# Performance work log

Measured on AMD Instinct MI355X. Metric: run time of the kernel, lower is better.

The kernel has to match this reference:

```python
import jax, jax.numpy as jnp
import numpy as np

B, L, NC, REG_MAX = 32, 8400, 15, 16
EPS_IOU = 0.1  # RotatedIoULoss eps (clamp min)


def _cross2(a, b):
    return a[..., 0] * b[..., 1] - a[..., 1] * b[..., 0]


def _box2corners(box):
    # box [...,5] = (x, y, w, h, alpha) -> corners [...,4,2], consistent cyclic order
    x, y, w, h, a = (box[..., i] for i in range(5))
    xo = jnp.array([0.5, -0.5, -0.5, 0.5], box.dtype)
    yo = jnp.array([-0.5, -0.5, 0.5, 0.5], box.dtype)
    px = w[..., None] * xo  # [...,4]
    py = h[..., None] * yo
    c, s = jnp.cos(a)[..., None], jnp.sin(a)[..., None]
    rx = c * px - s * py + x[..., None]
    ry = s * px + c * py + y[..., None]
    return jnp.stack([rx, ry], axis=-1)


def _box_intersection(c1, c2):
    # segment-segment intersections between the 4 edges of each box -> [N,16,2], valid [N,16]
    p1 = c1[:, :, None, :]
    p2 = jnp.roll(c1, -1, axis=-2)[:, :, None, :]
    q1 = c2[:, None, :, :]
    q2 = jnp.roll(c2, -1, axis=-2)[:, None, :, :]
    d1, d2, r = p2 - p1, q2 - q1, q1 - p1
    den = _cross2(d1, d2)
    safe = jnp.where(jnp.abs(den) < 1e-12, jnp.ones_like(den), den)
    t = _cross2(r, d2) / safe
    u = _cross2(r, d1) / safe
    valid = (jnp.abs(den) > 1e-12) & (t > 0) & (t < 1) & (u > 0) & (u < 1)
    pts = p1 + t[..., None] * d1
    pts = jnp.where(valid[..., None], pts, jnp.zeros_like(pts))
    N = c1.shape[0]
    return pts.reshape(N, 16, 2), valid.reshape(N, 16)


def _points_in_box(pts, corners):
    # pts [N,4,2] inside rotated box given by corners [N,4,2] (projection test)
    a = corners[:, 0:1]
    ab = corners[:, 1:2] - a
    ad = corners[:, 3:4] - a
    ap = pts - a
    pab = jnp.sum(ap * ab, -1)
    pad = jnp.sum(ap * ad, -1)
    nab = jnp.sum(ab * ab, -1)
    nad = jnp.sum(ad * ad, -1)
    return (pab >= 0) & (pab <= nab) & (pad >= 0) & (pad <= nad)


def _sorted_poly_area(verts, mask):
    # sort candidate vertices CCW around the centroid of valid ones, shoelace area
    mf = mask.astype(verts.dtype)
    nv = jnp.maximum(mf.sum(-1, keepdims=True), 1.0)  # [N,1]
    mean = (verts * mf[..., None]).sum(-2, keepdims=True) / nv[..., None]
    rel = verts - mean
    ang = jnp.where(mask, jnp.arctan2(rel[..., 1], rel[..., 0]), 1e6)
    order = jnp.argsort(ang, axis=-1)
    sv = jnp.take_along_axis(verts, order[..., None], axis=-2)
    sm = jnp.take_along_axis(mask, order, axis=-1)
    sv = jnp.where(sm[..., None], sv, sv[..., :1, :])  # pad invalid with first vertex
    nxt = jnp.roll(sv, -1, axis=-2)
    return 0.5 * jnp.abs(jnp.sum(sv[..., 0] * nxt[..., 1] - nxt[..., 0] * sv[..., 1], axis=-1))


def diff_iou_rotated_2d(box1, box2):
    # box1, box2: [N,5] -> iou [N]
    c1, c2 = _box2corners(box1), _box2corners(box2)
    ipts, ivalid = _box_intersection(c1, c2)
    m1 = _points_in_box(c1, c2)
    m2 = _points_in_box(c2, c1)
    verts = jnp.concatenate([c1, c2, ipts], axis=-2)   # [N,24,2]
    mask = jnp.concatenate([m1, m2, ivalid], axis=-1)  # [N,24]
    inter = _sorted_poly_area(verts, mask)
    area1 = box1[..., 2] * box1[..., 3]
    area2 = box2[..., 2] * box2[..., 3]
    return inter / (area1 + area2 - inter + 1e-9)


def setup_inputs() -> dict:
    key = jax.random.key(0)
    ks = jax.random.split(key, 8)
    wh_off = jnp.array([0.0, 0.0, 0.2, 0.2], jnp.float32)
    pred_bboxes = jax.random.uniform(ks[0], (B, L, 4), jnp.float32) + wh_off
    target_bboxes = jax.random.uniform(ks[1], (B, L, 4), jnp.float32) + wh_off
    pred_angles = 0.5 * jax.random.normal(ks[2], (B, L, 1), jnp.float32)      # radians
    target_angles = 90.0 * jax.random.uniform(ks[3], (B, L, 1), jnp.float32)  # degrees
    pred_dist = jax.random.normal(ks[4], (B, L, (REG_MAX + 1) * 4), jnp.float32)
    target_scores = jax.random.uniform(ks[5], (B, L, NC), jnp.float32)
    fg_mask = jax.random.bernoulli(ks[6], 0.25, (B, L))
    tss = jnp.sum(target_scores.sum(-1) * fg_mask.astype(jnp.float32))[None]
    anchor_points = jax.random.uniform(ks[7], (L, 2), jnp.float32)
    return {"pred_dist": pred_dist, "pred_bboxes": pred_bboxes, "pred_angles": pred_angles,
            "anchor_points": anchor_points, "target_bboxes": target_bboxes,
            "target_angles": target_angles, "target_scores": target_scores,
            "target_scores_sum": tss, "fg_mask": fg_mask}


def reference(pred_dist, pred_bboxes, pred_angles, anchor_points, target_bboxes,
              target_angles, target_scores, target_scores_sum, fg_mask):
    mf = fg_mask.astype(pred_bboxes.dtype).reshape(-1)          # [B*L]
    num_pos = mf.sum()
    pi = jnp.asarray(np.pi, pred_bboxes.dtype)
    pred_R = jnp.concatenate([pred_bboxes, pred_angles], -1).reshape(-1, 5)
    tgt_R = jnp.concatenate([target_bboxes, target_angles / 180.0 * pi], -1).reshape(-1, 5)
    ious = jnp.maximum(diff_iou_rotated_2d(pred_R, tgt_R), EPS_IOU)  # clamp(min=eps)
    bbox_weight = target_scores.sum(-1).reshape(-1)             # [B*L]
    loss_elem = (1.0 - ious) * bbox_weight * mf                 # masked per-anchor loss
    lsum = loss_elem.sum()
    lmean = lsum / jnp.maximum(num_pos, 1.0)
    loss_iou = jnp.where(target_scores_sum[0] == 0, lsum, lmean)
    loss_iou = jnp.where(num_pos > 0, loss_iou, 0.0)
    loss_dfl = pred_dist.sum() * 0.0
    return (loss_iou, loss_dfl)
```

## Files before the change

kernel.cpp:

```cpp
#include <hip/hip_runtime.h>
#include <math.h>

#define NCLS 15


__global__ void zero_ws_kernel(float* ws) {
    if (threadIdx.x < 2) ws[threadIdx.x] = 0.0f;
}

__global__ __launch_bounds__(256) void rbox_iou_kernel(
    const float* __restrict__ pred_bboxes,
    const float* __restrict__ pred_angles,
    const float* __restrict__ target_bboxes,
    const float* __restrict__ target_angles,
    const float* __restrict__ target_scores,
    const int*   __restrict__ fg_mask,
    float* __restrict__ ws,
    int n)
{
    const int i = blockIdx.x * blockDim.x + threadIdx.x;
    float loss = 0.0f, cnt = 0.0f;

    if (i < n && fg_mask[i] != 0) {
        cnt = 1.0f;

        const float4 pb = reinterpret_cast<const float4*>(pred_bboxes)[i];
        const float4 tb = reinterpret_cast<const float4*>(target_bboxes)[i];
        const float pa = pred_angles[i];
        const float ta = (target_angles[i] / 180.0f) * (float)M_PI;

        float c1x[4], c1y[4], c2x[4], c2y[4];
        {
            const float xo[4] = { 0.5f, -0.5f, -0.5f, 0.5f };
            const float yo[4] = { -0.5f, -0.5f, 0.5f, 0.5f };
            float cs = cosf(pa), sn = sinf(pa);
#pragma unroll
            for (int k = 0; k < 4; ++k) {
                float px = pb.z * xo[k], py = pb.w * yo[k];
                c1x[k] = cs * px - sn * py + pb.x;
                c1y[k] = sn * px + cs * py + pb.y;
            }
            cs = cosf(ta); sn = sinf(ta);
#pragma unroll
            for (int k = 0; k < 4; ++k) {
                float px = tb.z * xo[k], py = tb.w * yo[k];
                c2x[k] = cs * px - sn * py + tb.x;
                c2y[k] = sn * px + cs * py + tb.y;
            }
        }

        float vx[24], vy[24];
        bool  vm[24];

        {
            const float ax = c2x[0], ay = c2y[0];
            const float abx = c2x[1] - ax, aby = c2y[1] - ay;
            const float adx = c2x[3] - ax, ady = c2y[3] - ay;
            const float nab = abx * abx + aby * aby;
            const float nad = adx * adx + ady * ady;
#pragma unroll
            for (int k = 0; k < 4; ++k) {
                float apx = c1x[k] - ax, apy = c1y[k] - ay;
                float pab = apx * abx + apy * aby;
                float pad = apx * adx + apy * ady;
                vx[k] = c1x[k]; vy[k] = c1y[k];
                vm[k] = (pab >= 0.0f) && (pab <= nab) && (pad >= 0.0f) && (pad <= nad);
            }
        }
        {
            const float ax = c1x[0], ay = c1y[0];
            const float abx = c1x[1] - ax, aby = c1y[1] - ay;
            const float adx = c1x[3] - ax, ady = c1y[3] - ay;
            const float nab = abx * abx + aby * aby;
            const float nad = adx * adx + ady * ady;
#pragma unroll
            for (int k = 0; k < 4; ++k) {
                float apx = c2x[k] - ax, apy = c2y[k] - ay;
                float pab = apx * abx + apy * aby;
                float pad = apx * adx + apy * ady;
                vx[4 + k] = c2x[k]; vy[4 + k] = c2y[k];
                vm[4 + k] = (pab >= 0.0f) && (pab <= nab) && (pad >= 0.0f) && (pad <= nad);
            }
        }
#pragma unroll
        for (int a = 0; a < 4; ++a) {
            const float p1x = c1x[a], p1y = c1y[a];
            const float d1x = c1x[(a + 1) & 3] - p1x;
            const float d1y = c1y[(a + 1) & 3] - p1y;
#pragma unroll
            for (int b = 0; b < 4; ++b) {
                const float q1x = c2x[b], q1y = c2y[b];
                const float d2x = c2x[(b + 1) & 3] - q1x;
                const float d2y = c2y[(b + 1) & 3] - q1y;
                const float rx = q1x - p1x, ry = q1y - p1y;
                const float den = d1x * d2y - d1y * d2x;
                const float safe = (fabsf(den) < 1e-12f) ? 1.0f : den;
                const float t = (rx * d2y - ry * d2x) / safe;
                const float u = (rx * d1y - ry * d1x) / safe;
                const bool val = (fabsf(den) > 1e-12f) &&
                                 (t > 0.0f) && (t < 1.0f) &&
                                 (u > 0.0f) && (u < 1.0f);
                const int idx = 8 + a * 4 + b;
                vx[idx] = val ? (p1x + t * d1x) : 0.0f;
                vy[idx] = val ? (p1y + t * d1y) : 0.0f;
                vm[idx] = val;
            }
        }

        float sx = 0.0f, sy = 0.0f, nvf = 0.0f;
#pragma unroll
        for (int k = 0; k < 24; ++k) {
            sx  += vm[k] ? vx[k] : 0.0f;
            sy  += vm[k] ? vy[k] : 0.0f;
            nvf += vm[k] ? 1.0f : 0.0f;
        }
        const float nv = fmaxf(nvf, 1.0f);
        const float mx = sx / nv, my = sy / nv;

        float ang[24];
#pragma unroll
        for (int k = 0; k < 24; ++k) {
            const float rx = vx[k] - mx, ry = vy[k] - my;
            const float d = fabsf(rx) + fabsf(ry);
            const float a = rx / d;
            float p = (ry >= 0.0f) ? (1.0f - a) : (3.0f + a);
            if (d == 0.0f) p = 0.0f;
            ang[k] = vm[k] ? p : INFINITY;
        }

        float minA = INFINITY, mnx = 0.0f, mny = 0.0f;
#pragma unroll
        for (int k = 0; k < 24; ++k) {
            const bool t = ang[k] < minA;
            minA = t ? ang[k] : minA;
            mnx  = t ? vx[k]  : mnx;
            mny  = t ? vy[k]  : mny;
        }

        float total = 0.0f;
#pragma unroll
        for (int a = 0; a < 24; ++a) {
            const float ai = ang[a];
            float bestA = INFINITY;
            float bx = mnx, by = mny;
#pragma unroll
            for (int b = 0; b < 24; ++b) {
                if (b == a) continue;
                const float aj = ang[b];
                const bool gt = (b > a) ? (aj >= ai) : (aj > ai);
                const bool take = gt && (aj < bestA);
                bestA = take ? aj : bestA;
                bx = take ? vx[b] : bx;
                by = take ? vy[b] : by;
            }
            if (ai < INFINITY)
                total += vx[a] * by - bx * vy[a];
        }
        const float inter = 0.5f * fabsf(total);

        const float area1 = pb.z * pb.w;
        const float area2 = tb.z * tb.w;
        float iou = inter / (area1 + area2 - inter + 1e-9f);
        iou = fmaxf(iou, 0.1f);

        float w = 0.0f;
#pragma unroll
        for (int k = 0; k < NCLS; ++k) w += target_scores[i * NCLS + k];

        loss = (1.0f - iou) * w;
    }

#pragma unroll
    for (int off = 32; off > 0; off >>= 1) {
        loss += __shfl_down(loss, off, 64);
        cnt  += __shfl_down(cnt,  off, 64);
    }
    __shared__ float sl[4], sc[4];
    const int lane = threadIdx.x & 63;
    const int wid  = threadIdx.x >> 6;
    if (lane == 0) { sl[wid] = loss; sc[wid] = cnt; }
    __syncthreads();
    if (threadIdx.x == 0) {
        const float L = sl[0] + sl[1] + sl[2] + sl[3];
        const float C = sc[0] + sc[1] + sc[2] + sc[3];
        atomicAdd(&ws[0], L);
        atomicAdd(&ws[1], C);
    }
}

__global__ void finalize_kernel(const float* __restrict__ ws,
                                const float* __restrict__ tss,
                                float* __restrict__ out)
{
    const float lsum = ws[0];
    const float npos = ws[1];
    const float lmean = lsum / fmaxf(npos, 1.0f);
    float li = (tss[0] == 0.0f) ? lsum : lmean;
    li = (npos > 0.0f) ? li : 0.0f;
    out[0] = li;
    out[1] = 0.0f;
}

extern "C" void kernel_launch(void* const* d_in, const int* in_sizes, int n_in,
                              void* d_out, int out_size, void* d_ws, size_t ws_size,
                              hipStream_t stream) {
    const float* pred_bboxes   = (const float*)d_in[1];
    const float* pred_angles   = (const float*)d_in[2];
    const float* target_bboxes = (const float*)d_in[4];
    const float* target_angles = (const float*)d_in[5];
    const float* target_scores = (const float*)d_in[6];
    const float* tss           = (const float*)d_in[7];
    const int*   fg_mask       = (const int*)d_in[8];

    float* ws  = (float*)d_ws;
    float* out = (float*)d_out;

    const int n = in_sizes[8];
    const int blocks = (n + 255) / 256;

    zero_ws_kernel<<<1, 64, 0, stream>>>(ws);
    rbox_iou_kernel<<<blocks, 256, 0, stream>>>(
        pred_bboxes, pred_angles, target_bboxes, target_angles,
        target_scores, fg_mask, ws, n);
    finalize_kernel<<<1, 1, 0, stream>>>(ws, tss, out);
}
```

Before: 164.2 us.

## Compact foreground anchors and replace selection-based vertex ordering with bitonic sort

```diff
diff --git a/kernel.cpp b/kernel.cpp
--- a/kernel.cpp
+++ b/kernel.cpp
@@ -2,11 +2,50 @@
 #include <math.h>
 
 #define NCLS 15
+#define NV 24
 
 
 __global__ void zero_ws_kernel(float* ws) {
-    if (threadIdx.x < 2) ws[threadIdx.x] = 0.0f;
-}
+    if (threadIdx.x == 0) { ws[0] = 0.0f; ((int*)ws)[1] = 0; }
+}
+
+__global__ __launch_bounds__(256) void compact_kernel(
+    const int* __restrict__ fg_mask, int n,
+    int* __restrict__ cnt, int* __restrict__ idxbuf)
+{
+    const int i = blockIdx.x * 256 + threadIdx.x;
+    const bool pos = (i < n) && (fg_mask[i] != 0);
+    const unsigned long long b = __ballot(pos);
+    const int lane = threadIdx.x & 63;
+    const int wid  = threadIdx.x >> 6;
+    const int prefix = __popcll(b & ((1ULL << lane) - 1ULL));
+    const int wtotal = __popcll(b);
+
+    __shared__ int wbase[4];
+    if (lane == 0) wbase[wid] = wtotal;
+    __syncthreads();
+    if (threadIdx.x == 0) {
+        const int t0 = wbase[0], t1 = wbase[1], t2 = wbase[2], t3 = wbase[3];
+        const int base = atomicAdd(cnt, t0 + t1 + t2 + t3);
+        wbase[0] = base;
+        wbase[1] = base + t0;
+        wbase[2] = base + t0 + t1;
+        wbase[3] = base + t0 + t1 + t2;
+    }
+    __syncthreads();
+    if (pos) idxbuf[wbase[wid] + prefix] = i;
+}
+
+#define CSWAP(A, B)                                                       \
+    {                                                                     \
+        const float ka = ang[A], kb = ang[B];                             \
+        const bool sw = kb < ka;                                          \
+        ang[A] = sw ? kb : ka; ang[B] = sw ? ka : kb;                     \
+        const float xa = vx[A], xb = vx[B];                               \
+        vx[A] = sw ? xb : xa; vx[B] = sw ? xa : xb;                       \
+        const float ya = vy[A], yb = vy[B];                               \
+        vy[A] = sw ? yb : ya; vy[B] = sw ? ya : yb;                       \
+    }
 
 __global__ __launch_bounds__(256) void rbox_iou_kernel(
     const float* __restrict__ pred_bboxes,
@@ -14,15 +53,18 @@
     const float* __restrict__ target_bboxes,
     const float* __restrict__ target_angles,
     const float* __restrict__ target_scores,
-    const int*   __restrict__ fg_mask,
-    float* __restrict__ ws,
-    int n)
+    const int*   __restrict__ cnt,
+    const int*   __restrict__ idxbuf,
+    float* __restrict__ ws)
 {
-    const int i = blockIdx.x * blockDim.x + threadIdx.x;
-    float loss = 0.0f, cnt = 0.0f;
-
-    if (i < n && fg_mask[i] != 0) {
-        cnt = 1.0f;
+    const int count = *cnt;
+    if ((int)(blockIdx.x * 256) >= count) return;
+
+    const int j = blockIdx.x * 256 + threadIdx.x;
+    float loss = 0.0f;
+
+    if (j < count) {
+        const int i = idxbuf[j];
 
         const float4 pb = reinterpret_cast<const float4*>(pred_bboxes)[i];
         const float4 tb = reinterpret_cast<const float4*>(target_bboxes)[i];
@@ -36,21 +78,21 @@
             float cs = cosf(pa), sn = sinf(pa);
 #pragma unroll
             for (int k = 0; k < 4; ++k) {
-                float px = pb.z * xo[k], py = pb.w * yo[k];
+                const float px = pb.z * xo[k], py = pb.w * yo[k];
                 c1x[k] = cs * px - sn * py + pb.x;
                 c1y[k] = sn * px + cs * py + pb.y;
             }
             cs = cosf(ta); sn = sinf(ta);
 #pragma unroll
             for (int k = 0; k < 4; ++k) {
-                float px = tb.z * xo[k], py = tb.w * yo[k];
+                const float px = tb.z * xo[k], py = tb.w * yo[k];
                 c2x[k] = cs * px - sn * py + tb.x;
                 c2y[k] = sn * px + cs * py + tb.y;
             }
         }
 
-        float vx[24], vy[24];
-        bool  vm[24];
+        float vx[NV], vy[NV];
+        bool  vm[NV];
 
         {
             const float ax = c2x[0], ay = c2y[0];
@@ -60,9 +102,9 @@
             const float nad = adx * adx + ady * ady;
 #pragma unroll
             for (int k = 0; k < 4; ++k) {
-                float apx = c1x[k] - ax, apy = c1y[k] - ay;
-                float pab = apx * abx + apy * aby;
-                float pad = apx * adx + apy * ady;
+                const float apx = c1x[k] - ax, apy = c1y[k] - ay;
+                const float pab = apx * abx + apy * aby;
+                const float pad = apx * adx + apy * ady;
                 vx[k] = c1x[k]; vy[k] = c1y[k];
                 vm[k] = (pab >= 0.0f) && (pab <= nab) && (pad >= 0.0f) && (pad <= nad);
             }
@@ -75,9 +117,9 @@
             const float nad = adx * adx + ady * ady;
 #pragma unroll
             for (int k = 0; k < 4; ++k) {
-                float apx = c2x[k] - ax, apy = c2y[k] - ay;
-                float pab = apx * abx + apy * aby;
-                float pad = apx * adx + apy * ady;
+                const float apx = c2x[k] - ax, apy = c2y[k] - ay;
+                const float pab = apx * abx + apy * aby;
+                const float pad = apx * adx + apy * ady;
                 vx[4 + k] = c2x[k]; vy[4 + k] = c2y[k];
                 vm[4 + k] = (pab >= 0.0f) && (pab <= nab) && (pad >= 0.0f) && (pad <= nad);
             }
@@ -109,7 +151,7 @@
 
         float sx = 0.0f, sy = 0.0f, nvf = 0.0f;
 #pragma unroll
-        for (int k = 0; k < 24; ++k) {
+        for (int k = 0; k < NV; ++k) {
             sx  += vm[k] ? vx[k] : 0.0f;
             sy  += vm[k] ? vy[k] : 0.0f;
             nvf += vm[k] ? 1.0f : 0.0f;
@@ -117,9 +159,9 @@
         const float nv = fmaxf(nvf, 1.0f);
         const float mx = sx / nv, my = sy / nv;
 
-        float ang[24];
-#pragma unroll
-        for (int k = 0; k < 24; ++k) {
+        float ang[NV];
+#pragma unroll
+        for (int k = 0; k < NV; ++k) {
             const float rx = vx[k] - mx, ry = vy[k] - my;
             const float d = fabsf(rx) + fabsf(ry);
             const float a = rx / d;
@@ -128,33 +170,34 @@
             ang[k] = vm[k] ? p : INFINITY;
         }
 
-        float minA = INFINITY, mnx = 0.0f, mny = 0.0f;
-#pragma unroll
-        for (int k = 0; k < 24; ++k) {
-            const bool t = ang[k] < minA;
-            minA = t ? ang[k] : minA;
-            mnx  = t ? vx[k]  : mnx;
-            mny  = t ? vy[k]  : mny;
-        }
-
+#pragma unroll
+        for (int p = 1; p < 32; p <<= 1) {
+#pragma unroll
+            for (int k = p; k >= 1; k >>= 1) {
+#pragma unroll
+                for (int jj = k & (p - 1); jj + k < 32; jj += 2 * k) {
+#pragma unroll
+                    for (int ii = 0; ii < k; ++ii) {
+                        if (ii + jj + k < 32 &&
+                            ((ii + jj) / (2 * p)) == ((ii + jj + k) / (2 * p))) {
+                            if (ii + jj + k < NV) {
+                                CSWAP(ii + jj, ii + jj + k);
+                            }
+                        }
+                    }
+                }
+            }
+        }
+
+        const float v0x = vx[0], v0y = vy[0];
         float total = 0.0f;
 #pragma unroll
-        for (int a = 0; a < 24; ++a) {
-            const float ai = ang[a];
-            float bestA = INFINITY;
-            float bx = mnx, by = mny;
-#pragma unroll
-            for (int b = 0; b < 24; ++b) {
-                if (b == a) continue;
-                const float aj = ang[b];
-                const bool gt = (b > a) ? (aj >= ai) : (aj > ai);
-                const bool take = gt && (aj < bestA);
-                bestA = take ? aj : bestA;
-                bx = take ? vx[b] : bx;
-                by = take ? vy[b] : by;
-            }
-            if (ai < INFINITY)
-                total += vx[a] * by - bx * vy[a];
+        for (int k = 0; k < NV; ++k) {
+            const bool vk = ang[k] < INFINITY;
+            const bool vn = (k < NV - 1) ? (ang[k + 1] < INFINITY) : false;
+            const float nx = vn ? vx[k + 1] : v0x;
+            const float ny = vn ? vy[k + 1] : v0y;
+            total += vk ? (vx[k] * ny - nx * vy[k]) : 0.0f;
         }
         const float inter = 0.5f * fabsf(total);
 
@@ -164,28 +207,23 @@
         iou = fmaxf(iou, 0.1f);
 
         float w = 0.0f;
-#pragma unroll
-        for (int k = 0; k < NCLS; ++k) w += target_scores[i * NCLS + k];
+        const float* sp = target_scores + (size_t)i * NCLS;
+#pragma unroll
+        for (int k = 0; k < NCLS; ++k) w += sp[k];
 
         loss = (1.0f - iou) * w;
     }
 
 #pragma unroll
-    for (int off = 32; off > 0; off >>= 1) {
+    for (int off = 32; off > 0; off >>= 1)
         loss += __shfl_down(loss, off, 64);
-        cnt  += __shfl_down(cnt,  off, 64);
-    }
-    __shared__ float sl[4], sc[4];
+    __shared__ float sl[4];
     const int lane = threadIdx.x & 63;
     const int wid  = threadIdx.x >> 6;
-    if (lane == 0) { sl[wid] = loss; sc[wid] = cnt; }
+    if (lane == 0) sl[wid] = loss;
     __syncthreads();
-    if (threadIdx.x == 0) {
-        const float L = sl[0] + sl[1] + sl[2] + sl[3];
-        const float C = sc[0] + sc[1] + sc[2] + sc[3];
-        atomicAdd(&ws[0], L);
-        atomicAdd(&ws[1], C);
-    }
+    if (threadIdx.x == 0)
+        atomicAdd(&ws[0], sl[0] + sl[1] + sl[2] + sl[3]);
 }
 
 __global__ void finalize_kernel(const float* __restrict__ ws,
@@ -193,7 +231,7 @@
                                 float* __restrict__ out)
 {
     const float lsum = ws[0];
-    const float npos = ws[1];
+    const float npos = (float)((const int*)ws)[1];
     const float lmean = lsum / fmaxf(npos, 1.0f);
     float li = (tss[0] == 0.0f) ? lsum : lmean;
     li = (npos > 0.0f) ? li : 0.0f;
@@ -212,15 +250,18 @@
     const float* tss           = (const float*)d_in[7];
     const int*   fg_mask       = (const int*)d_in[8];
 
-    float* ws  = (float*)d_ws;
-    float* out = (float*)d_out;
+    float* ws     = (float*)d_ws;
+    int*   cnt    = (int*)d_ws + 1;
+    int*   idxbuf = (int*)d_ws + 16;
+    float* out    = (float*)d_out;
 
     const int n = in_sizes[8];
     const int blocks = (n + 255) / 256;
 
     zero_ws_kernel<<<1, 64, 0, stream>>>(ws);
+    compact_kernel<<<blocks, 256, 0, stream>>>(fg_mask, n, cnt, idxbuf);
     rbox_iou_kernel<<<blocks, 256, 0, stream>>>(
         pred_bboxes, pred_angles, target_bboxes, target_angles,
-        target_scores, fg_mask, ws, n);
+        target_scores, cnt, idxbuf, ws);
     finalize_kernel<<<1, 1, 0, stream>>>(ws, tss, out);
 }
```

After: 152.3 us. 1.08x faster.
